# Kernel optimization log

Measured on AMD Instinct MI355X. Metric: run time of the kernel, lower is better.

Reference implementation:

```python
import jax, jax.numpy as jnp
import numpy as np

# ---- Mamba2 config (matches init_kwargs) ----
D_MODEL = 256
D_STATE = 64
D_CONV = 4
EXPAND = 4
HEADDIM = 64
CHUNK = 64
D_INNER = EXPAND * D_MODEL          # 1024
NHEADS = D_INNER // HEADDIM         # 16
CONV_DIM = D_INNER + 2 * D_STATE    # 1152
D_IN_PROJ = 2 * D_INNER + 2 * D_STATE + NHEADS  # 2192
BATCH = 4
SEQLEN = 4096


def setup_inputs() -> dict:
    key = jax.random.key(0)
    ks = jax.random.split(key, 8)
    return {
        "u": jax.random.normal(ks[0], (BATCH, SEQLEN, D_MODEL), jnp.float32),
        "in_proj_w": jax.random.normal(ks[1], (D_IN_PROJ, D_MODEL), jnp.float32) * 0.02,
        "conv_w": jax.random.normal(ks[2], (CONV_DIM, 1, D_CONV), jnp.float32) * 0.2,
        "conv_b": jnp.zeros((CONV_DIM,), jnp.float32),
        "dt_bias": jax.random.normal(ks[3], (NHEADS,), jnp.float32) * 0.1,
        "A_log": jax.random.normal(ks[4], (NHEADS,), jnp.float32) * 0.1,
        "D": jax.random.normal(ks[5], (NHEADS,), jnp.float32) * 0.1,
        "norm_w": jnp.ones((D_INNER,), jnp.float32),
        "out_proj_w": jax.random.normal(ks[6], (D_MODEL, D_INNER), jnp.float32) * 0.02,
    }


def _segsum_exp(x):
    """exp(segsum(x)) for x: (..., T). Lower-triangular, zero above diagonal.
    segsum[i, j] = sum_{k=j+1..i} x[k] = cumsum[i] - cumsum[j] (for i >= j)."""
    T = x.shape[-1]
    cs = jnp.cumsum(x, axis=-1)
    seg = cs[..., :, None] - cs[..., None, :]
    mask = jnp.tril(jnp.ones((T, T), dtype=bool))
    return jnp.where(mask, jnp.exp(seg), 0.0)


def _ssd(x, A, B, C, chunk):
    """SSD chunked scan.
    x: (b, l, h, p)  A: (b, l, h)  B, C: (b, l, n) (shared across heads)."""
    b, l, h, p = x.shape
    c = l // chunk
    xc = x.reshape(b, c, chunk, h, p)
    Ac = A.reshape(b, c, chunk, h).transpose(0, 3, 1, 2)  # (b, h, c, l)
    Bc = B.reshape(b, c, chunk, -1)
    Cc = C.reshape(b, c, chunk, -1)

    A_cs = jnp.cumsum(Ac, axis=-1)                         # (b, h, c, l)
    L = _segsum_exp(Ac)                                    # (b, h, c, l, l)
    # Intra-chunk (diagonal block) output
    Y_diag = jnp.einsum('bcln,bcsn,bhcls,bcshp->bclhp', Cc, Bc, L, xc)

    # Per-chunk states
    decay_states = jnp.exp(A_cs[..., -1:] - A_cs)          # (b, h, c, l)
    states = jnp.einsum('bcln,bhcl,bclhp->bchpn', Bc, decay_states, xc)
    states = jnp.concatenate([jnp.zeros_like(states[:, :1]), states], axis=1)

    # Inter-chunk recurrence via segsum over chunk-level decays
    A_last = jnp.pad(A_cs[..., -1], ((0, 0), (0, 0), (1, 0)))  # (b, h, c+1)
    decay_chunk = _segsum_exp(A_last)                          # (b, h, c+1, c+1)
    new_states = jnp.einsum('bhzc,bchpn->bzhpn', decay_chunk, states)
    states_prev, final_state = new_states[:, :-1], new_states[:, -1]

    # State -> output (off-diagonal contribution)
    state_decay_out = jnp.exp(A_cs)                        # (b, h, c, l)
    Y_off = jnp.einsum('bcln,bchpn,bhcl->bclhp', Cc, states_prev, state_decay_out)

    Y = (Y_diag + Y_off).reshape(b, l, h, p)
    return Y, final_state


def _silu(x):
    return x * jax.nn.sigmoid(x)


def reference(u, in_proj_w, conv_w, conv_b, dt_bias, A_log, D, norm_w, out_proj_w):
    b, l, _ = u.shape
    A = -jnp.exp(A_log)                                    # (h,)

    zxbcdt = u @ in_proj_w.T                               # (b, l, D_IN_PROJ)
    z = zxbcdt[..., :D_INNER]
    xBC = zxbcdt[..., D_INNER:D_INNER + CONV_DIM]
    dt = jax.nn.softplus(zxbcdt[..., -NHEADS:] + dt_bias)  # (b, l, h)

    # Causal depthwise conv1d (kernel D_CONV, left padding)
    xp = jnp.pad(xBC, ((0, 0), (D_CONV - 1, 0), (0, 0)))
    conv = conv_b
    for w in range(D_CONV):
        conv = conv + xp[:, w:w + l, :] * conv_w[:, 0, w]
    xBC = _silu(conv)

    x = xBC[..., :D_INNER].reshape(b, l, NHEADS, HEADDIM)
    Bm = xBC[..., D_INNER:D_INNER + D_STATE]
    Cm = xBC[..., -D_STATE:]

    y, _final_state = _ssd(x * dt[..., None], A * dt, Bm, Cm, CHUNK)
    y = y + x * D[:, None]
    y = y.reshape(b, l, D_INNER)

    # Gated RMSNorm
    y = y * _silu(z)
    y = y * jax.lax.rsqrt(jnp.mean(y * y, axis=-1, keepdims=True) + 1e-5) * norm_w

    return y @ out_proj_w.T                                # (b, l, d_model)
```

## Files before the change

### kernel.cpp

```cpp
#include <hip/hip_runtime.h>
#include <math.h>

#define BATCH   4
#define SEQLEN  4096
#define DMODEL  256
#define DINNER  1024
#define NHEADS  16
#define HEADDIM 64
#define DSTATE  64
#define CONVDIM 1152
#define DPROJ   2192
#define NCHUNK  64
#define CHUNK   64
#define ROWS    (BATCH*SEQLEN)
#define NPAD1   2304
#define TS      72

typedef unsigned short u16;
using frag  = __attribute__((ext_vector_type(8))) short;
using f32x4 = __attribute__((ext_vector_type(4))) float;
using u32x4 = __attribute__((ext_vector_type(4))) unsigned int;

static __device__ __forceinline__ float bf2f(u16 u) {
    return __uint_as_float(((unsigned int)u) << 16);
}
static __device__ __forceinline__ u16 f2bf(float f) {
    unsigned int x = __float_as_uint(f);
    x += 0x7fffu + ((x >> 16) & 1u);
    return (u16)(x >> 16);
}
static __device__ __forceinline__ void nt_store16(void* p, uint4 v) {
    u32x4 t = {v.x, v.y, v.z, v.w};
    __builtin_nontemporal_store(t, (u32x4*)p);
}

__global__ __launch_bounds__(256) void cvt_bf16(const float* __restrict__ in,
                                                u16* __restrict__ out,
                                                int total4, int valid_rows, int colshift)
{
    const int i = blockIdx.x * 256 + threadIdx.x;
    if (i >= total4) return;
    const int e = i * 4;
    const int row = e >> colshift;
    ushort4 o;
    if (row < valid_rows) {
        float4 v = *(const float4*)(in + e);
        o.x = f2bf(v.x); o.y = f2bf(v.y); o.z = f2bf(v.z); o.w = f2bf(v.w);
    } else {
        o.x = 0; o.y = 0; o.z = 0; o.w = 0;
    }
    *(ushort4*)(out + e) = o;
}

template<int KTOT, bool C_BF, bool SCALE_A>
__global__ __launch_bounds__(256) void gemm_mfma(const u16* __restrict__ A,
                                                 const u16* __restrict__ W,
                                                 void* __restrict__ Cp,
                                                 int N,
                                                 const float* __restrict__ normv,
                                                 const float* __restrict__ nw)
{
    __shared__ u16 pool[128*136];
    u16* As = pool;
    u16* Ws = pool + 128*64;

    const int m0 = blockIdx.y * 128;
    const int n0 = blockIdx.x * 128;
    const int tid = threadIdx.x;
    const int lane = tid & 63;
    const int w  = tid >> 6;
    const int wr = w >> 1, wc = w & 1;

    const int srow = tid >> 3;
    const int scol = (tid & 7) * 8;
    const int ssw  = scol ^ ((srow & 7) * 8);

    const int lrow = lane & 15;
    const int kgrp = lane >> 4;
    const int swz  = (lrow & 7) * 8;

    float ascale[4];
    if constexpr (SCALE_A) {
        #pragma unroll
        for (int it = 0; it < 4; ++it)
            ascale[it] = rsqrtf(normv[m0 + it*32 + srow] * (1.f/1024.f) + 1e-5f);
    }

    f32x4 acc[4][4] = {};

    uint4 ra[4], rw[4];
    #pragma unroll
    for (int it = 0; it < 4; ++it) {
        const int r = it*32 + srow;
        ra[it] = *(const uint4*)(A + (size_t)(m0 + r)*KTOT + scol);
        rw[it] = *(const uint4*)(W + (size_t)(n0 + r)*KTOT + scol);
    }

    for (int kt = 0; kt < KTOT; kt += 64) {
        __syncthreads();
        #pragma unroll
        for (int it = 0; it < 4; ++it) {
            const int r = it*32 + srow;
            if constexpr (SCALE_A) {
                uint4 v = ra[it];
                unsigned int* pw = (unsigned int*)&v;
                const float* nwp = nw + kt + scol;
                #pragma unroll
                for (int q = 0; q < 4; ++q) {
                    const float lo = bf2f((u16)(pw[q] & 0xffff)) * ascale[it] * nwp[2*q];
                    const float hi = bf2f((u16)(pw[q] >> 16))    * ascale[it] * nwp[2*q+1];
                    pw[q] = (unsigned int)f2bf(lo) | ((unsigned int)f2bf(hi) << 16);
                }
                *(uint4*)&As[r*64 + ssw] = v;
            } else {
                *(uint4*)&As[r*64 + ssw] = ra[it];
            }
            *(uint4*)&Ws[r*64 + ssw] = rw[it];
        }
        __syncthreads();
        if (kt + 64 < KTOT) {
            #pragma unroll
            for (int it = 0; it < 4; ++it) {
                const int r = it*32 + srow;
                ra[it] = *(const uint4*)(A + (size_t)(m0 + r)*KTOT + kt + 64 + scol);
                rw[it] = *(const uint4*)(W + (size_t)(n0 + r)*KTOT + kt + 64 + scol);
            }
        }
        #pragma unroll
        for (int ks = 0; ks < 2; ++ks) {
            const int kx = (ks*32 + kgrp*8) ^ swz;
            frag af[4], bf[4];
            #pragma unroll
            for (int i = 0; i < 4; ++i)
                af[i] = *(const frag*)&As[(wr*64 + i*16 + lrow)*64 + kx];
            #pragma unroll
            for (int j = 0; j < 4; ++j)
                bf[j] = *(const frag*)&Ws[(wc*64 + j*16 + lrow)*64 + kx];
            #pragma unroll
            for (int i = 0; i < 4; ++i)
                #pragma unroll
                for (int j = 0; j < 4; ++j)
                    acc[i][j] = __builtin_amdgcn_mfma_f32_16x16x32_bf16(af[i], bf[j], acc[i][j], 0, 0, 0);
        }
    }

    if constexpr (C_BF) {
        __syncthreads();
        #pragma unroll
        for (int i = 0; i < 4; ++i)
            #pragma unroll
            for (int j = 0; j < 4; ++j)
                #pragma unroll
                for (int r = 0; r < 4; ++r)
                    pool[(wr*64 + i*16 + kgrp*4 + r)*136 + wc*64 + j*16 + lrow] =
                        f2bf(acc[i][j][r]);
        __syncthreads();
        #pragma unroll
        for (int q = 0; q < 8; ++q) {
            const int f  = q*2048 + tid*8;
            const int rl = f >> 7;
            const int cl = f & 127;
            const int col = n0 + cl;
            if (col < N)
                nt_store16((u16*)Cp + (size_t)(m0 + rl)*N + col,
                           *(const uint4*)&pool[rl*136 + cl]);
        }
    } else {
        #pragma unroll
        for (int i = 0; i < 4; ++i) {
            #pragma unroll
            for (int j = 0; j < 4; ++j) {
                const int col = n0 + wc*64 + j*16 + lrow;
                if (col < N) {
                    #pragma unroll
                    for (int r = 0; r < 4; ++r) {
                        const int row = m0 + wr*64 + i*16 + kgrp*4 + r;
                        __builtin_nontemporal_store(acc[i][j][r],
                            (float*)Cp + (size_t)row * N + col);
                    }
                }
            }
        }
    }
}

__global__ __launch_bounds__(256) void conv_kernel(const u16* __restrict__ zxbcdt,
                                                   const float* __restrict__ conv_w,
                                                   const float* __restrict__ conv_b,
                                                   u16* __restrict__ xconv)
{
    const int idx = blockIdx.x * 256 + threadIdx.x;
    const int ch  = idx % CONVDIM;
    const int row = idx / CONVDIM;
    const int l   = row & (SEQLEN-1);
    const int b   = row >> 12;

    float acc = conv_b[ch];
    #pragma unroll
    for (int w = 0; w < 4; ++w) {
        const int ls = l - 3 + w;
        if (ls >= 0) {
            acc += bf2f(zxbcdt[(size_t)(b*SEQLEN + ls) * DPROJ + DINNER + ch]) * conv_w[ch*4 + w];
        }
    }
    __builtin_nontemporal_store(f2bf(acc / (1.f + __expf(-acc))), xconv + idx);
}

__global__ __launch_bounds__(256) void ssd_phaseA(const u16* __restrict__ xconv,
                                                  const u16* __restrict__ zxbcdt,
                                                  const float* __restrict__ dt_bias,
                                                  const float* __restrict__ A_log,
                                                  u16* __restrict__ ybuf,
                                                  u16* __restrict__ statesT,
                                                  float* __restrict__ acs_g,
                                                  float* __restrict__ asum_g)
{
    const int h = blockIdx.x, c = blockIdx.y, b = blockIdx.z;
    const int tid = threadIdx.x;
    const int lane = tid & 63;
    const int w = tid >> 6;
    const int l0 = c * CHUNK;

    __shared__ u16 CtM[64*TS];
    __shared__ u16 Bt [64*TS];
    __shared__ u16 BtT[64*TS];
    __shared__ u16 xdtT[64*TS];
    __shared__ float a_cs[64];
    __shared__ float a_dt[64];

    if (w == 0) {
        const float raw = bf2f(zxbcdt[(size_t)(b*SEQLEN + l0 + lane)*DPROJ + (DPROJ - NHEADS) + h])
                        + dt_bias[h];
        const float sp = (raw > 20.f) ? raw : log1pf(__expf(raw));
        a_dt[lane] = sp;
        float v = -__expf(A_log[h]) * sp;
        #pragma unroll
        for (int o = 1; o < 64; o <<= 1) {
            float t = __shfl_up(v, o, 64);
            if (lane >= o) v += t;
        }
        a_cs[lane] = v;
    }
    __syncthreads();
    const float a_last = a_cs[63];

    {
        const int j  = tid >> 2;
        const int q0 = (tid & 3) * 16;
        const u16* rp = xconv + (size_t)(b*SEQLEN + l0 + j) * CONVDIM;
        const float dtv = a_dt[j];
        const float dec = __expf(a_last - a_cs[j]);

        *(uint4*)&CtM[j*TS + q0]     = *(const uint4*)(rp + DINNER + DSTATE + q0);
        *(uint4*)&CtM[j*TS + q0 + 8] = *(const uint4*)(rp + DINNER + DSTATE + q0 + 8);

        uint4 b0 = *(const uint4*)(rp + DINNER + q0);
        uint4 b1 = *(const uint4*)(rp + DINNER + q0 + 8);
        *(uint4*)&Bt[j*TS + q0]     = b0;
        *(uint4*)&Bt[j*TS + q0 + 8] = b1;
        unsigned int bw[8] = {b0.x, b0.y, b0.z, b0.w, b1.x, b1.y, b1.z, b1.w};
        #pragma unroll
        for (int s = 0; s < 8; ++s) {
            const int n0 = q0 + 2*s, n1 = n0 + 1;
            BtT[n0*TS + (j ^ (n0 & 0x38))] = f2bf(bf2f((u16)(bw[s] & 0xffff)) * dec);
            BtT[n1*TS + (j ^ (n1 & 0x38))] = f2bf(bf2f((u16)(bw[s] >> 16))    * dec);
        }

        uint4 x0 = *(const uint4*)(rp + h*HEADDIM + q0);
        uint4 x1 = *(const uint4*)(rp + h*HEADDIM + q0 + 8);
        unsigned int xw[8] = {x0.x, x0.y, x0.z, x0.w, x1.x, x1.y, x1.z, x1.w};
        #pragma unroll
        for (int s = 0; s < 8; ++s) {
            const int p0 = q0 + 2*s, p1 = p0 + 1;
            xdtT[p0*TS + (j ^ (p0 & 0x38))] = f2bf(bf2f((u16)(xw[s] & 0xffff)) * dtv);
            xdtT[p1*TS + (j ^ (p1 & 0x38))] = f2bf(bf2f((u16)(xw[s] >> 16))    * dtv);
        }
    }
    __syncthreads();

    const int lrow = lane & 15;
    const int kgrp = lane >> 4;

    f32x4 accG[4] = {};
    #pragma unroll
    for (int ks = 0; ks < 2; ++ks) {
        frag a = *(const frag*)&CtM[(w*16 + lrow)*TS + ks*32 + kgrp*8];
        #pragma unroll
        for (int cf = 0; cf < 4; ++cf) {
            frag bb = *(const frag*)&Bt[(cf*16 + lrow)*TS + ks*32 + kgrp*8];
            accG[cf] = __builtin_amdgcn_mfma_f32_16x16x32_bf16(a, bb, accG[cf], 0, 0, 0);
        }
    }

    {
        float aj[4];
        #pragma unroll
        for (int cf = 0; cf < 4; ++cf) aj[cf] = a_cs[cf*16 + lrow];
        #pragma unroll
        for (int r = 0; r < 4; ++r) {
            const int i = w*16 + kgrp*4 + r;
            const float ai = a_cs[i];
            #pragma unroll
            for (int cf = 0; cf < 4; ++cf) {
                const int jcol = cf*16 + lrow;
                const float g = (jcol <= i) ? accG[cf][r] * __expf(ai - aj[cf]) : 0.f;
                CtM[i*TS + jcol] = f2bf(g);
            }
        }
    }

    f32x4 accY[4] = {};
    #pragma unroll
    for (int ks = 0; ks < 2; ++ks) {
        frag a = *(const frag*)&CtM[(w*16 + lrow)*TS + ks*32 + kgrp*8];
        #pragma unroll
        for (int cf = 0; cf < 4; ++cf) {
            const int p = cf*16 + lrow;
            frag bb = *(const frag*)&xdtT[p*TS + ((ks*32 + kgrp*8) ^ (p & 0x38))];
            accY[cf] = __builtin_amdgcn_mfma_f32_16x16x32_bf16(a, bb, accY[cf], 0, 0, 0);
        }
    }
    #pragma unroll
    for (int r = 0; r < 4; ++r) {
        const int i = w*16 + kgrp*4 + r;
        #pragma unroll
        for (int cf = 0; cf < 4; ++cf)
            CtM[i*TS + cf*16 + lrow] = f2bf(accY[cf][r]);
    }

    f32x4 accS[4] = {};
    #pragma unroll
    for (int ks = 0; ks < 2; ++ks) {
        const int pr = w*16 + lrow;
        frag a = *(const frag*)&xdtT[pr*TS + ((ks*32 + kgrp*8) ^ (pr & 0x38))];
        #pragma unroll
        for (int cf = 0; cf < 4; ++cf) {
            const int n = cf*16 + lrow;
            frag bb = *(const frag*)&BtT[n*TS + ((ks*32 + kgrp*8) ^ (n & 0x38))];
            accS[cf] = __builtin_amdgcn_mfma_f32_16x16x32_bf16(a, bb, accS[cf], 0, 0, 0);
        }
    }
    __syncthreads();
    #pragma unroll
    for (int r = 0; r < 4; ++r) {
        const int p = w*16 + kgrp*4 + r;
        #pragma unroll
        for (int cf = 0; cf < 4; ++cf)
            xdtT[p*TS + cf*16 + lrow] = f2bf(accS[cf][r]);
    }
    __syncthreads();

    {
        const int rr = tid >> 2;
        const int q  = (tid & 3) * 16;
        u16* yg = ybuf + (size_t)(b*SEQLEN + l0 + rr)*DINNER + h*HEADDIM + q;
        nt_store16(yg,     *(const uint4*)&CtM[rr*TS + q]);
        nt_store16(yg + 8, *(const uint4*)&CtM[rr*TS + q + 8]);
        u16* sg = statesT + (((size_t)b*NCHUNK + c)*NHEADS + h)*4096 + tid*16;
        nt_store16(sg,     *(const uint4*)&xdtT[rr*TS + q]);
        nt_store16(sg + 8, *(const uint4*)&xdtT[rr*TS + q + 8]);
    }

    if (tid < 64) acs_g[(((size_t)b*NCHUNK + c)*NHEADS + h)*CHUNK + tid] = a_cs[tid];
    if (tid == 0) asum_g[((size_t)b*NHEADS + h)*NCHUNK + c] = a_last;
}

__global__ __launch_bounds__(256) void ssd_scan(u16* __restrict__ statesT,
                                                const float* __restrict__ asum_g)
{
    const int gid = blockIdx.x;
    const int s = gid & 15;
    const int h = (gid >> 4) & (NHEADS-1);
    const int b = gid >> 8;
    const int elem = s*256 + threadIdx.x;

    const float* as = asum_g + ((size_t)b*NHEADS + h)*NCHUNK;
    float P = 0.f;
    for (int c = 0; c < NCHUNK; ++c) {
        const size_t idx = (((size_t)b*NCHUNK + c)*NHEADS + h)*4096 + elem;
        const float sv = bf2f(statesT[idx]);
        statesT[idx] = f2bf(P);
        P = P * __expf(as[c]) + sv;
    }
}

__global__ __launch_bounds__(256) void ssd_phaseC(const u16* __restrict__ xconv,
                                                  const u16* __restrict__ zxbcdt,
                                                  const u16* __restrict__ statesT,
                                                  const float* __restrict__ acs_g,
                                                  const float* __restrict__ Dvec,
                                                  u16* __restrict__ ybuf,
                                                  float* __restrict__ normbuf)
{
    const int h = blockIdx.x, c = blockIdx.y, b = blockIdx.z;
    const int tid = threadIdx.x;
    const int lane = tid & 63;
    const int w = tid >> 6;
    const int l0 = c * CHUNK;

    __shared__ u16 Ct [64*TS];
    __shared__ u16 SpT[64*TS];
    __shared__ float a_cs[64];

    if (tid < 64) a_cs[tid] = acs_g[(((size_t)b*NCHUNK + c)*NHEADS + h)*CHUNK + tid];
    {
        const int r  = tid >> 2;
        const int q0 = (tid & 3) * 16;
        const u16* cp = xconv + (size_t)(b*SEQLEN + l0 + r)*CONVDIM + DINNER + DSTATE;
        *(uint4*)&Ct[r*TS + q0]     = *(const uint4*)(cp + q0);
        *(uint4*)&Ct[r*TS + q0 + 8] = *(const uint4*)(cp + q0 + 8);
        const u16* spg = statesT + (((size_t)b*NCHUNK + c)*NHEADS + h)*4096 + r*64;
        *(uint4*)&SpT[r*TS + q0]     = *(const uint4*)(spg + q0);
        *(uint4*)&SpT[r*TS + q0 + 8] = *(const uint4*)(spg + q0 + 8);
    }
    __syncthreads();

    const int lrow = lane & 15;
    const int kgrp = lane >> 4;

    f32x4 acc[4] = {};
    #pragma unroll
    for (int ks = 0; ks < 2; ++ks) {
        frag a = *(const frag*)&Ct[(w*16 + lrow)*TS + ks*32 + kgrp*8];
        #pragma unroll
        for (int cf = 0; cf < 4; ++cf) {
            frag bb = *(const frag*)&SpT[(cf*16 + lrow)*TS + ks*32 + kgrp*8];
            acc[cf] = __builtin_amdgcn_mfma_f32_16x16x32_bf16(a, bb, acc[cf], 0, 0, 0);
        }
    }

    const float Dh = Dvec[h];
    #pragma unroll
    for (int r = 0; r < 4; ++r) {
        const int i = w*16 + kgrp*4 + r;
        const int l = l0 + i;
        const float e = __expf(a_cs[i]);
        const u16* xr = xconv  + (size_t)(b*SEQLEN + l)*CONVDIM + h*HEADDIM;
        const u16* zr = zxbcdt + (size_t)(b*SEQLEN + l)*DPROJ   + h*HEADDIM;
        u16* yp = ybuf + (size_t)(b*SEQLEN + l)*DINNER + h*HEADDIM;
        float ssq = 0.f;
        #pragma unroll
        for (int cf = 0; cf < 4; ++cf) {
            const int p = cf*16 + lrow;
            const float yv = bf2f(yp[p]) + e*acc[cf][r] + bf2f(xr[p])*Dh;
            const float zv = bf2f(zr[p]);
            const float fin = yv * (zv / (1.f + __expf(-zv)));
            ssq += fin * fin;
            yp[p] = f2bf(fin);
        }
        #pragma unroll
        for (int o = 1; o < 16; o <<= 1) ssq += __shfl_xor(ssq, o, 16);
        if (lrow == 0) atomicAdd(normbuf + (size_t)(b*SEQLEN + l), ssq);
    }
}

extern "C" void kernel_launch(void* const* d_in, const int* in_sizes, int n_in,
                              void* d_out, int out_size, void* d_ws, size_t ws_size,
                              hipStream_t stream)
{
    const float* u          = (const float*)d_in[0];
    const float* in_proj_w  = (const float*)d_in[1];
    const float* conv_w     = (const float*)d_in[2];
    const float* conv_b     = (const float*)d_in[3];
    const float* dt_bias    = (const float*)d_in[4];
    const float* A_log      = (const float*)d_in[5];
    const float* Dvec       = (const float*)d_in[6];
    const float* norm_w     = (const float*)d_in[7];
    const float* out_proj_w = (const float*)d_in[8];
    float* out = (float*)d_out;

    float* acs     = (float*)d_ws;
    float* asum    = acs  + (size_t)BATCH*NCHUNK*NHEADS*CHUNK;
    float* normbuf = asum + (size_t)BATCH*NHEADS*NCHUNK;
    u16* zxbcdt = (u16*)(normbuf + (size_t)ROWS);
    u16* xconv  = zxbcdt + (size_t)ROWS*DPROJ;
    u16* ybuf   = xconv  + (size_t)ROWS*CONVDIM;
    u16* states = ybuf   + (size_t)ROWS*DINNER;
    u16* w2b    = states + (size_t)BATCH*NCHUNK*NHEADS*DSTATE*HEADDIM;
    u16* u_bf   = states;
    u16* w1b    = states + (size_t)ROWS*DMODEL;

    hipMemsetAsync(normbuf, 0, ROWS*sizeof(float), stream);

    cvt_bf16<<<(ROWS*DMODEL/4+255)/256, 256, 0, stream>>>(u, u_bf, ROWS*DMODEL/4, ROWS, 8);
    cvt_bf16<<<(NPAD1*DMODEL/4+255)/256, 256, 0, stream>>>(in_proj_w, w1b, NPAD1*DMODEL/4, DPROJ, 8);
    cvt_bf16<<<(DMODEL*DINNER/4+255)/256, 256, 0, stream>>>(out_proj_w, w2b, DMODEL*DINNER/4, DMODEL, 10);

    gemm_mfma<DMODEL, true, false><<<dim3(NPAD1/128, ROWS/128), 256, 0, stream>>>(
        u_bf, w1b, zxbcdt, DPROJ, nullptr, nullptr);

    conv_kernel<<<(ROWS*CONVDIM)/256, 256, 0, stream>>>(zxbcdt, conv_w, conv_b, xconv);
    ssd_phaseA<<<dim3(NHEADS, NCHUNK, BATCH), 256, 0, stream>>>(
        xconv, zxbcdt, dt_bias, A_log, ybuf, states, acs, asum);
    ssd_scan<<<BATCH*NHEADS*16, 256, 0, stream>>>(states, asum);
    ssd_phaseC<<<dim3(NHEADS, NCHUNK, BATCH), 256, 0, stream>>>(
        xconv, zxbcdt, states, acs, Dvec, ybuf, normbuf);

    gemm_mfma<DINNER, false, true><<<dim3(DMODEL/128, ROWS/128), 256, 0, stream>>>(
        ybuf, w2b, out, DMODEL, normbuf, norm_w);
}
```

Measured before the change: 424.2 us.

## Fuse input fp32-to-bf16 conversion into in_proj GEMM and swizzle block order

The first GEMM now reads the fp32 input directly and converts to bf16 while staging into shared memory, so the separate conversion kernel and its intermediate buffer go away. Block indices in both GEMMs and both SSD phase kernels are also remapped with an XCD-style swizzle (stride over groups of 8) so that neighbouring tiles land on the same chiplet for better L2 reuse. The fused path doubles the global read bytes for A per tile in the GEMM and adds conversion instructions to its inner loop.

```diff
diff --git a/kernel.cpp b/kernel.cpp
--- a/kernel.cpp
+++ b/kernel.cpp
@@ -29,6 +29,9 @@
     x += 0x7fffu + ((x >> 16) & 1u);
     return (u16)(x >> 16);
 }
+static __device__ __forceinline__ unsigned int pk2(float lo, float hi) {
+    return (unsigned int)f2bf(lo) | ((unsigned int)f2bf(hi) << 16);
+}
 static __device__ __forceinline__ void nt_store16(void* p, uint4 v) {
     u32x4 t = {v.x, v.y, v.z, v.w};
     __builtin_nontemporal_store(t, (u32x4*)p);
@@ -52,8 +55,8 @@
     *(ushort4*)(out + e) = o;
 }
 
-template<int KTOT, bool C_BF, bool SCALE_A>
-__global__ __launch_bounds__(256) void gemm_mfma(const u16* __restrict__ A,
+template<int KTOT, bool C_BF, bool SCALE_A, bool A_F32>
+__global__ __launch_bounds__(256) void gemm_mfma(const void* __restrict__ Ap,
                                                  const u16* __restrict__ W,
                                                  void* __restrict__ Cp,
                                                  int N,
@@ -64,8 +67,16 @@
     u16* As = pool;
     u16* Ws = pool + 128*64;
 
-    const int m0 = blockIdx.y * 128;
-    const int n0 = blockIdx.x * 128;
+    const int gx   = gridDim.x;
+    const int nwg  = gx * gridDim.y;
+    const int flat = blockIdx.y * gx + blockIdx.x;
+    const int swzb = (flat & 7) * (nwg >> 3) + (flat >> 3);
+    const int m0 = (swzb / gx) * 128;
+    const int n0 = (swzb % gx) * 128;
+
+    const float* Af = (const float*)Ap;
+    const u16*   Ab = (const u16*)Ap;
+
     const int tid = threadIdx.x;
     const int lane = tid & 63;
     const int w  = tid >> 6;
@@ -89,10 +100,16 @@
     f32x4 acc[4][4] = {};
 
     uint4 ra[4], rw[4];
+    float4 raf[4][2];
     #pragma unroll
     for (int it = 0; it < 4; ++it) {
         const int r = it*32 + srow;
-        ra[it] = *(const uint4*)(A + (size_t)(m0 + r)*KTOT + scol);
+        if constexpr (A_F32) {
+            raf[it][0] = *(const float4*)(Af + (size_t)(m0 + r)*KTOT + scol);
+            raf[it][1] = *(const float4*)(Af + (size_t)(m0 + r)*KTOT + scol + 4);
+        } else {
+            ra[it] = *(const uint4*)(Ab + (size_t)(m0 + r)*KTOT + scol);
+        }
         rw[it] = *(const uint4*)(W + (size_t)(n0 + r)*KTOT + scol);
     }
 
@@ -101,7 +118,14 @@
         #pragma unroll
         for (int it = 0; it < 4; ++it) {
             const int r = it*32 + srow;
-            if constexpr (SCALE_A) {
+            if constexpr (A_F32) {
+                uint4 v;
+                v.x = pk2(raf[it][0].x, raf[it][0].y);
+                v.y = pk2(raf[it][0].z, raf[it][0].w);
+                v.z = pk2(raf[it][1].x, raf[it][1].y);
+                v.w = pk2(raf[it][1].z, raf[it][1].w);
+                *(uint4*)&As[r*64 + ssw] = v;
+            } else if constexpr (SCALE_A) {
                 uint4 v = ra[it];
                 unsigned int* pw = (unsigned int*)&v;
                 const float* nwp = nw + kt + scol;
@@ -109,7 +133,7 @@
                 for (int q = 0; q < 4; ++q) {
                     const float lo = bf2f((u16)(pw[q] & 0xffff)) * ascale[it] * nwp[2*q];
                     const float hi = bf2f((u16)(pw[q] >> 16))    * ascale[it] * nwp[2*q+1];
-                    pw[q] = (unsigned int)f2bf(lo) | ((unsigned int)f2bf(hi) << 16);
+                    pw[q] = pk2(lo, hi);
                 }
                 *(uint4*)&As[r*64 + ssw] = v;
             } else {
@@ -122,7 +146,12 @@
             #pragma unroll
             for (int it = 0; it < 4; ++it) {
                 const int r = it*32 + srow;
-                ra[it] = *(const uint4*)(A + (size_t)(m0 + r)*KTOT + kt + 64 + scol);
+                if constexpr (A_F32) {
+                    raf[it][0] = *(const float4*)(Af + (size_t)(m0 + r)*KTOT + kt + 64 + scol);
+                    raf[it][1] = *(const float4*)(Af + (size_t)(m0 + r)*KTOT + kt + 64 + scol + 4);
+                } else {
+                    ra[it] = *(const uint4*)(Ab + (size_t)(m0 + r)*KTOT + kt + 64 + scol);
+                }
                 rw[it] = *(const uint4*)(W + (size_t)(n0 + r)*KTOT + kt + 64 + scol);
             }
         }
@@ -215,7 +244,12 @@
                                                   float* __restrict__ acs_g,
                                                   float* __restrict__ asum_g)
 {
-    const int h = blockIdx.x, c = blockIdx.y, b = blockIdx.z;
+    const int flat = blockIdx.x + NHEADS*(blockIdx.y + NCHUNK*blockIdx.z);
+    const int swzb = (flat & 7) * (BATCH*NCHUNK*NHEADS/8) + (flat >> 3);
+    const int h = swzb & (NHEADS-1);
+    const int c = (swzb >> 4) & (NCHUNK-1);
+    const int b = swzb >> 10;
+
     const int tid = threadIdx.x;
     const int lane = tid & 63;
     const int w = tid >> 6;
@@ -392,7 +426,12 @@
                                                   u16* __restrict__ ybuf,
                                                   float* __restrict__ normbuf)
 {
-    const int h = blockIdx.x, c = blockIdx.y, b = blockIdx.z;
+    const int flat = blockIdx.x + NHEADS*(blockIdx.y + NCHUNK*blockIdx.z);
+    const int swzb = (flat & 7) * (BATCH*NCHUNK*NHEADS/8) + (flat >> 3);
+    const int h = swzb & (NHEADS-1);
+    const int c = (swzb >> 4) & (NCHUNK-1);
+    const int b = swzb >> 10;
+
     const int tid = threadIdx.x;
     const int lane = tid & 63;
     const int w = tid >> 6;
@@ -477,17 +516,15 @@
     u16* ybuf   = xconv  + (size_t)ROWS*CONVDIM;
     u16* states = ybuf   + (size_t)ROWS*DINNER;
     u16* w2b    = states + (size_t)BATCH*NCHUNK*NHEADS*DSTATE*HEADDIM;
-    u16* u_bf   = states;
-    u16* w1b    = states + (size_t)ROWS*DMODEL;
+    u16* w1b    = states;
 
     hipMemsetAsync(normbuf, 0, ROWS*sizeof(float), stream);
 
-    cvt_bf16<<<(ROWS*DMODEL/4+255)/256, 256, 0, stream>>>(u, u_bf, ROWS*DMODEL/4, ROWS, 8);
     cvt_bf16<<<(NPAD1*DMODEL/4+255)/256, 256, 0, stream>>>(in_proj_w, w1b, NPAD1*DMODEL/4, DPROJ, 8);
     cvt_bf16<<<(DMODEL*DINNER/4+255)/256, 256, 0, stream>>>(out_proj_w, w2b, DMODEL*DINNER/4, DMODEL, 10);
 
-    gemm_mfma<DMODEL, true, false><<<dim3(NPAD1/128, ROWS/128), 256, 0, stream>>>(
-        u_bf, w1b, zxbcdt, DPROJ, nullptr, nullptr);
+    gemm_mfma<DMODEL, true, false, true><<<dim3(NPAD1/128, ROWS/128), 256, 0, stream>>>(
+        u, w1b, zxbcdt, DPROJ, nullptr, nullptr);
 
     conv_kernel<<<(ROWS*CONVDIM)/256, 256, 0, stream>>>(zxbcdt, conv_w, conv_b, xconv);
     ssd_phaseA<<<dim3(NHEADS, NCHUNK, BATCH), 256, 0, stream>>>(
@@ -496,6 +533,6 @@
     ssd_phaseC<<<dim3(NHEADS, NCHUNK, BATCH), 256, 0, stream>>>(
         xconv, zxbcdt, states, acs, Dvec, ybuf, normbuf);
 
-    gemm_mfma<DINNER, false, true><<<dim3(DMODEL/128, ROWS/128), 256, 0, stream>>>(
+    gemm_mfma<DINNER, false, true, false><<<dim3(DMODEL/128, ROWS/128), 256, 0, stream>>>(
         ybuf, w2b, out, DMODEL, normbuf, norm_w);
 }
```

Result: faster. 390.0 us (-8.1%).
